# Performance work log

Measured on AMD Instinct MI355X. Metric: run time of the kernel, lower is better.

The kernel has to match this reference:

```python
import jax, jax.numpy as jnp
import numpy as np

D = 256        # embedding_dim
K = 4096       # num_embeddings
DECAY = 0.99
EPS = 1e-05
COMMIT = 0.25


def setup_inputs() -> dict:
    key = jax.random.key(0)
    kx, ke = jax.random.split(key)
    x = jax.random.normal(kx, (32, 1024, D), dtype=jnp.float32)
    # variance_scaling(scale=1.0, mode='fan_in', distribution='uniform') on (D, K): fan_in = D
    limit = np.sqrt(3.0 / D).astype(np.float32)
    embeddings = jax.random.uniform(ke, (D, K), dtype=jnp.float32, minval=-limit, maxval=limit)
    return {
        'x': x,
        'embeddings': embeddings,
        'ema_counter': jnp.zeros((), jnp.float32),
        'ema_hidden_cluster': jnp.zeros((K,), jnp.float32),
        'ema_hidden_dw': jnp.zeros((D, K), jnp.float32),
    }


def reference(x, embeddings, ema_counter, ema_hidden_cluster, ema_hidden_dw):
    flat = x.reshape(-1, D)  # [N, D]
    # squared euclidean distance to each code: [N, K]
    distance = (jnp.sum(flat ** 2, axis=1, keepdims=True)
                - 2.0 * jnp.matmul(flat, embeddings)
                + jnp.sum(embeddings ** 2, axis=0, keepdims=True))
    encoding_indices = jnp.argmax(-distance, axis=1)           # [N]
    encodings = jax.nn.one_hot(encoding_indices, K, dtype=distance.dtype)  # [N, K]
    idx = encoding_indices.reshape(x.shape[:-1])               # [B, T]
    quantized = jnp.take(embeddings.T, idx, axis=0)            # [B, T, D]

    e_latent_loss = jnp.mean((quantized - x) ** 2)
    q_latent_loss = jnp.mean((quantized - x) ** 2)
    vq_loss = q_latent_loss + COMMIT * e_latent_loss

    # EMA codebook update (training=True path); debiased EMA per the module
    counter = ema_counter + 1.0
    bias = 1.0 - jnp.power(DECAY, counter)
    cluster_hidden = ema_hidden_cluster * DECAY + jnp.sum(encodings, axis=0) * (1.0 - DECAY)
    cluster_avg = cluster_hidden / bias                         # [K]
    dw = jnp.matmul(flat.T, encodings)                          # [D, K]
    dw_hidden = ema_hidden_dw * DECAY + dw * (1.0 - DECAY)
    dw_avg = dw_hidden / bias                                   # [D, K]
    n = jnp.sum(cluster_avg)
    cluster_norm = (cluster_avg + EPS) / (n + K * EPS) * n
    new_embeddings = dw_avg / cluster_norm[None, :]             # [D, K]

    avg_probs = jnp.mean(encodings, axis=0)
    perplexity = jnp.exp(-jnp.sum(avg_probs * jnp.log(avg_probs + 1e-10)))
    return quantized, vq_loss, perplexity, idx, new_embeddings
```

## Files before the change

kernel.cpp:

```cpp
#include <hip/hip_runtime.h>
#include <math.h>

#define N_TOK 32768
#define DIM   256
#define KCODE 4096

#define WS_E2      0
#define WS_COUNTS  4096
#define WS_LOSSP   8192
#define WS_SCAL    8448
#define WS_CNORM   8512
#define WS_IDX     12608
#define WS_EHS     307520
#define WS_DWT     1356096
#define WS_CARRYV  2404672
#define WS_CARRYI  2437440
#define WS_OFFS    2470208
#define WS_WOFF    2474304

#define OUT_Q      0
#define OUT_LOSS   8388608
#define OUT_PERP   8388609
#define OUT_IDX    8388610
#define OUT_EMB    8421378

#define EH_PLANE   1048576

typedef _Float16 f16x8 __attribute__((ext_vector_type(8)));
typedef _Float16 f16x4 __attribute__((ext_vector_type(4)));
typedef float    f32x4 __attribute__((ext_vector_type(4)));

__global__ void k_split_e(const float* __restrict__ emb, unsigned short* __restrict__ ehs_,
                          float* __restrict__ e2)
{
    __shared__ float tile[32][33];
    _Float16* ehs = (_Float16*)ehs_;
    int t  = threadIdx.x;
    int tx = t & 31, iy = t >> 5;
    int k0 = blockIdx.x * 32, d0 = blockIdx.y * 32;
#pragma unroll
    for (int j = 0; j < 4; ++j)
        tile[iy + 8 * j][tx] = emb[(size_t)(d0 + iy + 8 * j) * KCODE + k0 + tx];
    __syncthreads();
    int code = k0 + tx;
    size_t base = (size_t)(((code >> 8) * 8) + (d0 >> 5)) * 8192 + (code & 255) * 32 + iy * 4;
    f16x4 h1, h2;
    float ssq = 0.0f;
#pragma unroll
    for (int j = 0; j < 4; ++j) {
        float v = tile[iy * 4 + j][tx];
        ssq += v * v;
        _Float16 a = (_Float16)v;
        h1[j] = a;
        h2[j] = (_Float16)(v - (float)a);
    }
    *(f16x4*)(ehs + base)            = h1;
    *(f16x4*)(ehs + EH_PLANE + base) = h2;
    atomicAdd(&e2[code], ssq);
}

__global__ __launch_bounds__(256, 2)
void k_argmin(const float* __restrict__ x, const unsigned short* __restrict__ ehs_,
              const float* __restrict__ e2, int* __restrict__ idx_out,
              float* __restrict__ carryV, int* __restrict__ carryI,
              float* __restrict__ out_idxf, float* __restrict__ counts,
              float* __restrict__ lossp, float* __restrict__ out_q,
              int ct0, int phase)
{
    __shared__ __align__(16) _Float16 Ah[2][64][256];
    __shared__ float xsqp[64][8];
    __shared__ int   bis[64];

    const _Float16* ehs = (const _Float16*)ehs_;

    const int t    = threadIdx.x;
    const int lane = t & 63, w = t >> 6;
    const int lo   = lane & 15, q = lane >> 4;
    const int row0 = blockIdx.x * 64;

    {
        int m = t >> 3, kb = (t & 7) * 32;
        float ssq0 = 0.0f, ssq1 = 0.0f;
#pragma unroll
        for (int rr = 0; rr < 2; ++rr) {
            int mm = m + 32 * rr;
            const float* src = x + (size_t)(row0 + mm) * DIM + kb;
            float ss = 0.0f;
#pragma unroll
            for (int g = 0; g < 4; ++g) {
                f32x4 f0 = __builtin_nontemporal_load((const f32x4*)(src + g * 8));
                f32x4 f1 = __builtin_nontemporal_load((const f32x4*)(src + g * 8 + 4));
                f16x8 h1, h2;
#pragma unroll
                for (int j = 0; j < 4; ++j) {
                    ss += f0[j] * f0[j] + f1[j] * f1[j];
                    _Float16 a = (_Float16)f0[j];
                    h1[j] = a; h2[j] = (_Float16)(f0[j] - (float)a);
                    _Float16 b = (_Float16)f1[j];
                    h1[j + 4] = b; h2[j + 4] = (_Float16)(f1[j] - (float)b);
                }
                int grp = ((kb >> 3) + g) ^ (mm & 7);
                *(f16x8*)&Ah[0][mm][grp * 8] = h1;
                *(f16x8*)&Ah[1][mm][grp * 8] = h2;
            }
            if (rr == 0) ssq0 = ss; else ssq1 = ss;
        }
        xsqp[m][t & 7]      = ssq0;
        xsqp[m + 32][t & 7] = ssq1;
    }
    __syncthreads();

    float best[16];
    int   bidx[16];
#pragma unroll
    for (int s = 0; s < 16; ++s) { best[s] = 3.4e38f; bidx[s] = 0x40000000; }

    const _Float16* ehp1 = ehs + (size_t)(w * 64 + lo) * 32 + q * 8;
    const _Float16* ehp2 = ehp1 + EH_PLANE;

    f16x8 b1f[2][4], b2f[2][4];

    {
        const size_t so0 = (size_t)(ct0 * 8) * 8192;
#pragma unroll
        for (int nf = 0; nf < 4; ++nf) {
            b1f[0][nf] = *(const f16x8*)(ehp1 + so0 + nf * 512);
            b2f[0][nf] = *(const f16x8*)(ehp2 + so0 + nf * 512);
        }
    }

    for (int ct = ct0; ct < ct0 + 8; ++ct) {
        float e2r[4];
#pragma unroll
        for (int nf = 0; nf < 4; ++nf)
            e2r[nf] = e2[ct * 256 + w * 64 + nf * 16 + lo];

        f32x4 acc[4][4];
#pragma unroll
        for (int mf = 0; mf < 4; ++mf)
#pragma unroll
            for (int nf = 0; nf < 4; ++nf) acc[mf][nf] = (f32x4)0.0f;

#pragma unroll
        for (int ks = 0; ks < 8; ++ks) {
            const int cur = ks & 1, nxt = cur ^ 1;
            const int so  = ct * 8 + ks;

            if (ks < 7 || ct < ct0 + 7) {
                const size_t po = (size_t)(so + 1) * 8192;
#pragma unroll
                for (int nf = 0; nf < 4; ++nf) {
                    b1f[nxt][nf] = *(const f16x8*)(ehp1 + po + nf * 512);
                    b2f[nxt][nf] = *(const f16x8*)(ehp2 + po + nf * 512);
                }
            }
            __builtin_amdgcn_sched_barrier(0);

            const int agrp = ((ks * 4 + q) ^ (lo & 7)) * 8;
            f16x8 a1[4], a2[4];
#pragma unroll
            for (int mf = 0; mf < 4; ++mf)
                a2[mf] = *(const f16x8*)&Ah[1][mf * 16 + lo][agrp];
#pragma unroll
            for (int mf = 0; mf < 4; ++mf)
                a1[mf] = *(const f16x8*)&Ah[0][mf * 16 + lo][agrp];

#pragma unroll
            for (int nf = 0; nf < 4; ++nf) {
#pragma unroll
                for (int mf = 0; mf < 4; ++mf)
                    acc[mf][nf] = __builtin_amdgcn_mfma_f32_16x16x32_f16(a2[mf], b1f[cur][nf], acc[mf][nf], 0, 0, 0);
#pragma unroll
                for (int mf = 0; mf < 4; ++mf)
                    acc[mf][nf] = __builtin_amdgcn_mfma_f32_16x16x32_f16(a1[mf], b2f[cur][nf], acc[mf][nf], 0, 0, 0);
#pragma unroll
                for (int mf = 0; mf < 4; ++mf)
                    acc[mf][nf] = __builtin_amdgcn_mfma_f32_16x16x32_f16(a1[mf], b1f[cur][nf], acc[mf][nf], 0, 0, 0);
            }
        }

#pragma unroll
        for (int nf = 0; nf < 4; ++nf) {
            int ci = ct * 256 + w * 64 + nf * 16 + lo;
            float e2v = e2r[nf];
#pragma unroll
            for (int mf = 0; mf < 4; ++mf)
#pragma unroll
                for (int r = 0; r < 4; ++r) {
                    float dist = fmaf(-2.0f, acc[mf][nf][r], e2v);
                    int s = mf * 4 + r;
                    if (dist < best[s] || (dist == best[s] && ci < bidx[s])) {
                        best[s] = dist; bidx[s] = ci;
                    }
                }
        }
    }

    __syncthreads();
    float* rv = (float*)&Ah[0][0][0];
    int*   ri = (int*)(((char*)&Ah[0][0][0]) + 16384);
#pragma unroll
    for (int s = 0; s < 16; ++s) {
        int row = (s >> 2) * 16 + q * 4 + (s & 3);
        rv[row * 64 + w * 16 + lo] = best[s];
        ri[row * 64 + w * 16 + lo] = bidx[s];
    }
    __syncthreads();
    if (t < 64) {
        float bv; int bi;
        if (phase) { bv = carryV[row0 + t]; bi = carryI[row0 + t]; }
        else       { bv = 3.4e38f; bi = 0x40000000; }
        for (int jj = 0; jj < 64; ++jj) {
            int j = (jj + t) & 63;
            float v = rv[t * 64 + j];
            int  ii = ri[t * 64 + j];
            if (v < bv || (v == bv && ii < bi)) { bv = v; bi = ii; }
        }
        if (phase) {
            idx_out[row0 + t] = bi;
            out_idxf[row0 + t] = (float)bi;
            atomicAdd(&counts[bi], 1.0f);
            bis[t] = bi;
            float xsq = 0.0f;
#pragma unroll
            for (int j = 0; j < 8; ++j) xsq += xsqp[t][j];
            float lr = bv + xsq;
#pragma unroll
            for (int off = 32; off > 0; off >>= 1) lr += __shfl_down(lr, off, 64);
            if (t == 0) atomicAdd(&lossp[blockIdx.x & 255], lr);
        } else {
            carryV[row0 + t] = bv; carryI[row0 + t] = bi;
        }
    }
    if (phase) {
        __syncthreads();
        int r  = t >> 2, qs = t & 3;
        int k  = bis[r];
        float* dst = out_q + (size_t)(row0 + r) * DIM + qs * 64;
        const _Float16* ehb = ehs + (size_t)((k >> 8) * 8 + qs * 2) * 8192 + (k & 255) * 32;
#pragma unroll
        for (int dd = 0; dd < 2; ++dd) {
            const _Float16* p1 = ehb + dd * 8192;
            const _Float16* p2 = p1 + EH_PLANE;
#pragma unroll
            for (int g = 0; g < 4; ++g) {
                f16x8 h1 = *(const f16x8*)(p1 + g * 8);
                f16x8 h2 = *(const f16x8*)(p2 + g * 8);
                float4 o0, o1;
                o0.x = (float)h1[0] + (float)h2[0];
                o0.y = (float)h1[1] + (float)h2[1];
                o0.z = (float)h1[2] + (float)h2[2];
                o0.w = (float)h1[3] + (float)h2[3];
                o1.x = (float)h1[4] + (float)h2[4];
                o1.y = (float)h1[5] + (float)h2[5];
                o1.z = (float)h1[6] + (float)h2[6];
                o1.w = (float)h1[7] + (float)h2[7];
                *(float4*)(dst + dd * 32 + g * 8)     = o0;
                *(float4*)(dst + dd * 32 + g * 8 + 4) = o1;
            }
        }
    }
}

__global__ void k_scanfin(const float* __restrict__ counts, const float* __restrict__ lossp,
                          const float* __restrict__ ema_counter,
                          const float* __restrict__ ema_cluster,
                          int* __restrict__ offs, int* __restrict__ woff,
                          float* __restrict__ cnorm, float* __restrict__ scal,
                          float* __restrict__ out)
{
    __shared__ int   ps[256];
    __shared__ float red[256];
    int t = threadIdx.x;

    int local[16];
    int s = 0;
#pragma unroll
    for (int j = 0; j < 16; ++j) {
        local[j] = s;
        s += (int)counts[t * 16 + j];
    }
    ps[t] = s;
    __syncthreads();
    for (int off = 1; off < 256; off <<= 1) {
        int v = (t >= off) ? ps[t - off] : 0;
        __syncthreads();
        ps[t] += v;
        __syncthreads();
    }
    int base = (t > 0) ? ps[t - 1] : 0;
#pragma unroll
    for (int j = 0; j < 16; ++j) {
        int o = base + local[j];
        offs[t * 16 + j] = o;
        woff[t * 16 + j] = o;
    }

    float ls = lossp[t];
    float ent = 0.0f, casum = 0.0f;
    float ca[16];
#pragma unroll
    for (int j = 0; j < 16; ++j) {
        int k = j * 256 + t;
        float c = counts[k];
        float p = c * (1.0f / 32768.0f);
        ent += p * logf(p + 1e-10f);
        ca[j] = ema_cluster[k] * 0.99f + c * 0.01f;
        casum += ca[j];
    }
    __syncthreads();
    red[t] = ls; __syncthreads();
    for (int o = 128; o > 0; o >>= 1) { if (t < o) red[t] += red[t + o]; __syncthreads(); }
    float loss_tot = red[0]; __syncthreads();
    red[t] = ent; __syncthreads();
    for (int o = 128; o > 0; o >>= 1) { if (t < o) red[t] += red[t + o]; __syncthreads(); }
    float ent_tot = red[0]; __syncthreads();
    red[t] = casum; __syncthreads();
    for (int o = 128; o > 0; o >>= 1) { if (t < o) red[t] += red[t + o]; __syncthreads(); }
    float casum_tot = red[0]; __syncthreads();

    float bias = 1.0f - powf(0.99f, ema_counter[0] + 1.0f);
    float n = casum_tot / bias;
    float inv = n / (n + 4096.0f * 1e-5f);
#pragma unroll
    for (int j = 0; j < 16; ++j) {
        int k = j * 256 + t;
        cnorm[k] = (ca[j] / bias + 1e-5f) * inv;
    }
    if (t == 0) {
        out[OUT_LOSS] = 1.25f * loss_tot * (1.0f / (32768.0f * 256.0f));
        out[OUT_PERP] = expf(-ent_tot);
        scal[0] = bias;
    }
}

__global__ void k_scatter(const int* __restrict__ idx, int* __restrict__ woff,
                          int* __restrict__ rowlist)
{
    int n = blockIdx.x * 256 + threadIdx.x;
    int k = idx[n];
    int pos = atomicAdd(&woff[k], 1);
    rowlist[pos] = n;
}

__global__ void k_dw(const float* __restrict__ x, const int* __restrict__ rowlist,
                     const int* __restrict__ offs, const float* __restrict__ counts,
                     float* __restrict__ dwT)
{
    __shared__ __align__(16) float red[4][256];
    int k = blockIdx.x, t = threadIdx.x;
    int lane = t & 63, w = t >> 6;
    int start = offs[k];
    int cnt   = (int)counts[k];
    float4 acc = {0.0f, 0.0f, 0.0f, 0.0f};
    for (int j = w; j < cnt; j += 4) {
        int n = rowlist[start + j];
        float4 xv = *(const float4*)&x[(size_t)n * DIM + lane * 4];
        acc.x += xv.x; acc.y += xv.y; acc.z += xv.z; acc.w += xv.w;
    }
    *(float4*)&red[w][lane * 4] = acc;
    __syncthreads();
    float s = red[0][t] + red[1][t] + red[2][t] + red[3][t];
    dwT[(size_t)k * DIM + t] = s;
}

__global__ void k_newemb(const float* __restrict__ dwT, const float* __restrict__ ema_dw,
                         const float* __restrict__ cnorm, const float* __restrict__ scal,
                         float* __restrict__ out_emb)
{
    __shared__ float tile[32][33];
    int t = threadIdx.x;
    int tx = t & 31, iy = t >> 5;
    int k0 = blockIdx.x * 32, d0 = blockIdx.y * 32;
#pragma unroll
    for (int j = 0; j < 4; ++j)
        tile[iy + 8 * j][tx] = dwT[(size_t)(k0 + iy + 8 * j) * DIM + d0 + tx];
    __syncthreads();
    float inv_bias = 1.0f / scal[0];
    float cn = cnorm[k0 + tx];
#pragma unroll
    for (int j = 0; j < 4; ++j) {
        int d = d0 + iy + 8 * j;
        float dwv = tile[tx][iy + 8 * j];
        float hid = ema_dw[(size_t)d * KCODE + k0 + tx] * 0.99f + dwv * 0.01f;
        out_emb[(size_t)d * KCODE + k0 + tx] = hid * inv_bias / cn;
    }
}

extern "C" void kernel_launch(void* const* d_in, const int* in_sizes, int n_in,
                              void* d_out, int out_size, void* d_ws, size_t ws_size,
                              hipStream_t stream)
{
    const float* x           = (const float*)d_in[0];
    const float* emb         = (const float*)d_in[1];
    const float* ema_counter = (const float*)d_in[2];
    const float* ema_cluster = (const float*)d_in[3];
    const float* ema_dw      = (const float*)d_in[4];
    float* out = (float*)d_out;
    float* ws  = (float*)d_ws;

    float* e2     = ws + WS_E2;
    float* counts = ws + WS_COUNTS;
    float* lossp  = ws + WS_LOSSP;
    float* scal   = ws + WS_SCAL;
    float* cnorm  = ws + WS_CNORM;
    int*   idxw   = (int*)(ws + WS_IDX);
    unsigned short* ehs = (unsigned short*)(ws + WS_EHS);
    float* dwT    = ws + WS_DWT;
    float* carryV = ws + WS_CARRYV;
    int*   carryI = (int*)(ws + WS_CARRYI);
    int*   rowlist= (int*)(ws + WS_CARRYV);
    int*   offs   = (int*)(ws + WS_OFFS);
    int*   woff   = (int*)(ws + WS_WOFF);

    hipMemsetAsync(e2, 0, (size_t)WS_CNORM * sizeof(float), stream);

    k_split_e<<<dim3(128, 8), 256, 0, stream>>>(emb, ehs, e2);
    k_argmin<<<512, 256, 0, stream>>>(x, ehs, e2, idxw, carryV, carryI,
                                      out + OUT_IDX, counts, lossp, out + OUT_Q, 0, 0);
    k_argmin<<<512, 256, 0, stream>>>(x, ehs, e2, idxw, carryV, carryI,
                                      out + OUT_IDX, counts, lossp, out + OUT_Q, 8, 1);
    k_scanfin<<<1, 256, 0, stream>>>(counts, lossp, ema_counter, ema_cluster,
                                     offs, woff, cnorm, scal, out);
    k_scatter<<<128, 256, 0, stream>>>(idxw, woff, rowlist);
    k_dw<<<4096, 256, 0, stream>>>(x, rowlist, offs, counts, dwT);
    k_newemb<<<dim3(128, 8), 256, 0, stream>>>(dwT, ema_dw, cnorm, scal, out + OUT_EMB);
}
```

Before: 334.4 us.

## Move quantized output write into dw kernel and drop memset/atomics

The gather-and-write of quantized rows moves out of the phase-1 argmin kernel and into the per-code dw kernel. Each block reconstructs its code vector once in shared memory and writes it to every assigned row. The split-embedding kernel now loops over all dimension tiles per block, so e2 is written directly instead of through atomics. The memset is replaced by zeroing counts and loss partials inside the phase-0 argmin. This removes a launch, atomics and repeated gathers of the code planes, but the quantized writes become scattered by row.

```diff
diff --git a/kernel.cpp b/kernel.cpp
--- a/kernel.cpp
+++ b/kernel.cpp
@@ -34,29 +34,41 @@
                           float* __restrict__ e2)
 {
     __shared__ float tile[32][33];
+    __shared__ float ssq_red[8][32];
     _Float16* ehs = (_Float16*)ehs_;
     int t  = threadIdx.x;
     int tx = t & 31, iy = t >> 5;
-    int k0 = blockIdx.x * 32, d0 = blockIdx.y * 32;
-#pragma unroll
-    for (int j = 0; j < 4; ++j)
-        tile[iy + 8 * j][tx] = emb[(size_t)(d0 + iy + 8 * j) * KCODE + k0 + tx];
-    __syncthreads();
-    int code = k0 + tx;
-    size_t base = (size_t)(((code >> 8) * 8) + (d0 >> 5)) * 8192 + (code & 255) * 32 + iy * 4;
-    f16x4 h1, h2;
+    int k0 = blockIdx.x * 32;
     float ssq = 0.0f;
-#pragma unroll
-    for (int j = 0; j < 4; ++j) {
-        float v = tile[iy * 4 + j][tx];
-        ssq += v * v;
-        _Float16 a = (_Float16)v;
-        h1[j] = a;
-        h2[j] = (_Float16)(v - (float)a);
-    }
-    *(f16x4*)(ehs + base)            = h1;
-    *(f16x4*)(ehs + EH_PLANE + base) = h2;
-    atomicAdd(&e2[code], ssq);
+    for (int dt = 0; dt < 8; ++dt) {
+        int d0 = dt * 32;
+        __syncthreads();
+#pragma unroll
+        for (int j = 0; j < 4; ++j)
+            tile[iy + 8 * j][tx] = emb[(size_t)(d0 + iy + 8 * j) * KCODE + k0 + tx];
+        __syncthreads();
+        int code = k0 + tx;
+        size_t base = (size_t)(((code >> 8) * 8) + (d0 >> 5)) * 8192 + (code & 255) * 32 + iy * 4;
+        f16x4 h1, h2;
+#pragma unroll
+        for (int j = 0; j < 4; ++j) {
+            float v = tile[iy * 4 + j][tx];
+            ssq += v * v;
+            _Float16 a = (_Float16)v;
+            h1[j] = a;
+            h2[j] = (_Float16)(v - (float)a);
+        }
+        *(f16x4*)(ehs + base)            = h1;
+        *(f16x4*)(ehs + EH_PLANE + base) = h2;
+    }
+    ssq_red[iy][tx] = ssq;
+    __syncthreads();
+    if (iy == 0) {
+        float s = 0.0f;
+#pragma unroll
+        for (int j = 0; j < 8; ++j) s += ssq_red[j][tx];
+        e2[k0 + tx] = s;
+    }
 }
 
 __global__ __launch_bounds__(256, 2)
@@ -64,12 +76,10 @@
               const float* __restrict__ e2, int* __restrict__ idx_out,
               float* __restrict__ carryV, int* __restrict__ carryI,
               float* __restrict__ out_idxf, float* __restrict__ counts,
-              float* __restrict__ lossp, float* __restrict__ out_q,
-              int ct0, int phase)
+              float* __restrict__ lossp, int ct0, int phase)
 {
     __shared__ __align__(16) _Float16 Ah[2][64][256];
     __shared__ float xsqp[64][8];
-    __shared__ int   bis[64];
 
     const _Float16* ehs = (const _Float16*)ehs_;
 
@@ -77,6 +87,11 @@
     const int lane = t & 63, w = t >> 6;
     const int lo   = lane & 15, q = lane >> 4;
     const int row0 = blockIdx.x * 64;
+
+    if (!phase) {
+        if (blockIdx.x < 16)       counts[blockIdx.x * 256 + t] = 0.0f;
+        else if (blockIdx.x == 16 && t < 256) lossp[t] = 0.0f;
+    }
 
     {
         int m = t >> 3, kb = (t & 7) * 32;
@@ -220,7 +235,6 @@
             idx_out[row0 + t] = bi;
             out_idxf[row0 + t] = (float)bi;
             atomicAdd(&counts[bi], 1.0f);
-            bis[t] = bi;
             float xsq = 0.0f;
 #pragma unroll
             for (int j = 0; j < 8; ++j) xsq += xsqp[t][j];
@@ -230,34 +244,6 @@
             if (t == 0) atomicAdd(&lossp[blockIdx.x & 255], lr);
         } else {
             carryV[row0 + t] = bv; carryI[row0 + t] = bi;
-        }
-    }
-    if (phase) {
-        __syncthreads();
-        int r  = t >> 2, qs = t & 3;
-        int k  = bis[r];
-        float* dst = out_q + (size_t)(row0 + r) * DIM + qs * 64;
-        const _Float16* ehb = ehs + (size_t)((k >> 8) * 8 + qs * 2) * 8192 + (k & 255) * 32;
-#pragma unroll
-        for (int dd = 0; dd < 2; ++dd) {
-            const _Float16* p1 = ehb + dd * 8192;
-            const _Float16* p2 = p1 + EH_PLANE;
-#pragma unroll
-            for (int g = 0; g < 4; ++g) {
-                f16x8 h1 = *(const f16x8*)(p1 + g * 8);
-                f16x8 h2 = *(const f16x8*)(p2 + g * 8);
-                float4 o0, o1;
-                o0.x = (float)h1[0] + (float)h2[0];
-                o0.y = (float)h1[1] + (float)h2[1];
-                o0.z = (float)h1[2] + (float)h2[2];
-                o0.w = (float)h1[3] + (float)h2[3];
-                o1.x = (float)h1[4] + (float)h2[4];
-                o1.y = (float)h1[5] + (float)h2[5];
-                o1.z = (float)h1[6] + (float)h2[6];
-                o1.w = (float)h1[7] + (float)h2[7];
-                *(float4*)(dst + dd * 32 + g * 8)     = o0;
-                *(float4*)(dst + dd * 32 + g * 8 + 4) = o1;
-            }
         }
     }
 }
@@ -343,20 +329,29 @@
     rowlist[pos] = n;
 }
 
-__global__ void k_dw(const float* __restrict__ x, const int* __restrict__ rowlist,
-                     const int* __restrict__ offs, const float* __restrict__ counts,
-                     float* __restrict__ dwT)
-{
+__global__ void k_dw(const float* __restrict__ x, const unsigned short* __restrict__ ehs_,
+                     const int* __restrict__ rowlist, const int* __restrict__ offs,
+                     const float* __restrict__ counts, float* __restrict__ dwT,
+                     float* __restrict__ out_q)
+{
+    __shared__ __align__(16) float es[256];
     __shared__ __align__(16) float red[4][256];
+    const _Float16* ehs = (const _Float16*)ehs_;
     int k = blockIdx.x, t = threadIdx.x;
     int lane = t & 63, w = t >> 6;
+    size_t base = (size_t)(((k >> 8) * 8) + (t >> 5)) * 8192 + (k & 255) * 32 + (t & 31);
+    float e = (float)ehs[base] + (float)ehs[EH_PLANE + base];
+    es[t] = e;
     int start = offs[k];
     int cnt   = (int)counts[k];
+    __syncthreads();
+    float4 ev = *(const float4*)&es[lane * 4];
     float4 acc = {0.0f, 0.0f, 0.0f, 0.0f};
     for (int j = w; j < cnt; j += 4) {
         int n = rowlist[start + j];
         float4 xv = *(const float4*)&x[(size_t)n * DIM + lane * 4];
         acc.x += xv.x; acc.y += xv.y; acc.z += xv.z; acc.w += xv.w;
+        *(float4*)&out_q[(size_t)n * DIM + lane * 4] = ev;
     }
     *(float4*)&red[w][lane * 4] = acc;
     __syncthreads();
@@ -413,16 +408,14 @@
     int*   offs   = (int*)(ws + WS_OFFS);
     int*   woff   = (int*)(ws + WS_WOFF);
 
-    hipMemsetAsync(e2, 0, (size_t)WS_CNORM * sizeof(float), stream);
-
-    k_split_e<<<dim3(128, 8), 256, 0, stream>>>(emb, ehs, e2);
+    k_split_e<<<128, 256, 0, stream>>>(emb, ehs, e2);
     k_argmin<<<512, 256, 0, stream>>>(x, ehs, e2, idxw, carryV, carryI,
-                                      out + OUT_IDX, counts, lossp, out + OUT_Q, 0, 0);
+                                      out + OUT_IDX, counts, lossp, 0, 0);
     k_argmin<<<512, 256, 0, stream>>>(x, ehs, e2, idxw, carryV, carryI,
-                                      out + OUT_IDX, counts, lossp, out + OUT_Q, 8, 1);
+                                      out + OUT_IDX, counts, lossp, 8, 1);
     k_scanfin<<<1, 256, 0, stream>>>(counts, lossp, ema_counter, ema_cluster,
                                      offs, woff, cnorm, scal, out);
     k_scatter<<<128, 256, 0, stream>>>(idxw, woff, rowlist);
-    k_dw<<<4096, 256, 0, stream>>>(x, rowlist, offs, counts, dwT);
+    k_dw<<<4096, 256, 0, stream>>>(x, ehs, rowlist, offs, counts, dwT, out + OUT_Q);
     k_newemb<<<dim3(128, 8), 256, 0, stream>>>(dwT, ema_dw, cnorm, scal, out + OUT_EMB);
 }
```

Result: faster. 326.6 us (-2.3%).
